# Kernel tuning notes

Measured on AMD Instinct MI355X. Metric: run time of the kernel, lower is better.

## Reference

```python
import jax, jax.numpy as jnp
import numpy as np

B, NQ, NK = 32, 1, 4096
Q_SIZE = K_SIZE = 512
H = 256


def setup_inputs() -> dict:
    key = jax.random.key(0)
    ks = jax.random.split(key, 6)
    return {
        "queries": jax.random.normal(ks[0], (B, NQ, Q_SIZE), jnp.float32),
        "keys": jax.random.normal(ks[1], (B, NK, K_SIZE), jnp.float32),
        "values": jax.random.normal(ks[2], (B, NK, 1), jnp.float32),
        "W_q": jax.random.normal(ks[3], (Q_SIZE, H), jnp.float32) / np.sqrt(Q_SIZE),
        "W_k": jax.random.normal(ks[4], (K_SIZE, H), jnp.float32) / np.sqrt(K_SIZE),
        "w_v": jax.random.normal(ks[5], (H,), jnp.float32) / np.sqrt(H),
    }


def reference(queries, keys, values, W_q, W_k, w_v):
    # Project queries and keys to hidden dim
    q = jnp.einsum("bqd,dh->bqh", queries, W_q)            # [B, NQ, H]
    k = jnp.einsum("bkd,dh->bkh", keys, W_k)               # [B, NK, H]
    # Broadcast-add + tanh: [B, NQ, NK, H]
    features = jnp.tanh(q[:, :, None, :] + k[:, None, :, :])
    # Reduce hidden dim with w_v -> scores [B, NQ, NK]
    scores = jnp.einsum("bqkh,h->bqk", features, w_v)
    attn = jax.nn.softmax(scores, axis=-1)                 # [B, NQ, NK]
    # Module squeezes n_q dim (==1) and trailing value dim (==1)
    return attn[:, 0, :] * values[:, :, 0]                 # [B, NK]
```

## Files before the change

kernel.cpp:

```cpp
#include <hip/hip_runtime.h>
#include <cstdint>
#include <cstddef>

#define NB 32
#define NKEYS 4096
#define DQ 512
#define HDIM 256

#define BM 64
#define BK 64

typedef __attribute__((ext_vector_type(8))) short bf16x8;
typedef __attribute__((ext_vector_type(4))) float f32x4;

typedef __attribute__((address_space(1))) const unsigned int g_u32;
typedef __attribute__((address_space(3))) unsigned int l_u32;

__device__ __forceinline__ unsigned short f2bf(float f) {
    union { float f; unsigned u; } v; v.f = f;
    unsigned r = v.u + 0x7FFFu + ((v.u >> 16) & 1u);
    return (unsigned short)(r >> 16);
}

__device__ __forceinline__ float tanh_fast(float x) {
    float e = __expf(2.0f * x);
    return 1.0f - 2.0f / (e + 1.0f);
}

__device__ __forceinline__ void gload_lds16(const void* g, void* l) {
    __builtin_amdgcn_global_load_lds((g_u32*)g, (l_u32*)l, 16, 0, 0);
}

__global__ void k_prep_wkT(const float* __restrict__ Wk, unsigned short* __restrict__ WkT) {
    __shared__ unsigned short t[64][65];
    const int tid = threadIdx.x;
    const int dt = (blockIdx.x >> 2) << 6;
    const int ht = (blockIdx.x & 3) << 6;
    #pragma unroll
    for (int i = 0; i < 16; ++i) {
        int idx = tid + i * 256;
        int d = idx >> 6, h = idx & 63;
        t[d][h] = f2bf(Wk[(size_t)(dt + d) * HDIM + ht + h]);
    }
    __syncthreads();
    #pragma unroll
    for (int i = 0; i < 16; ++i) {
        int idx = tid + i * 256;
        int h = idx >> 6, d = idx & 63;
        WkT[(size_t)(ht + h) * DQ + dt + d] = t[d][h];
    }
}

__global__ void k_qproj(const float* __restrict__ q, const float* __restrict__ Wq,
                        float* __restrict__ qp) {
    __shared__ float qrow[DQ];
    __shared__ float part[256];
    const int blk = blockIdx.x;
    const int b = blk >> 2, hq = blk & 3;
    const int tid = threadIdx.x;
    qrow[tid]       = q[b * DQ + tid];
    qrow[tid + 256] = q[b * DQ + tid + 256];
    __syncthreads();
    const int h = (hq << 6) + (tid & 63);
    const int d0 = (tid >> 6) << 7;
    float s = 0.f;
    #pragma unroll 4
    for (int d = d0; d < d0 + 128; ++d)
        s += qrow[d] * Wq[d * HDIM + h];
    part[tid] = s;
    __syncthreads();
    if (tid < 64)
        qp[b * HDIM + (hq << 6) + tid] =
            part[tid] + part[tid + 64] + part[tid + 128] + part[tid + 192];
}

__global__ __launch_bounds__(256, 2) void k_scores(
        const float* __restrict__ keys, const unsigned short* __restrict__ WkT,
        const float* __restrict__ qp, const float* __restrict__ wv,
        float* __restrict__ scores) {
    __shared__ __align__(16) unsigned short As[2][BM * BK];
    __shared__ __align__(16) unsigned short Bs[2][HDIM * BK];
    float* s_rows = reinterpret_cast<float*>(&As[0][0]);

    const int tid  = threadIdx.x;
    const int lane = tid & 63;
    const int wid  = tid >> 6;
    const int row0 = blockIdx.x * BM;
    const int b    = row0 >> 12;
    const int l15  = lane & 15;
    const int l4   = lane >> 4;

    const int ar  = tid >> 4;
    const int ac4 = tid & 15;
    const float* aptr[4];
    int awoff[4];
    #pragma unroll
    for (int i = 0; i < 4; ++i) {
        const int row = ar + i * 16;
        aptr[i]  = keys + (size_t)(row0 + row) * DQ + ac4 * 4;
        awoff[i] = row * 128 + (((ac4 >> 1) ^ (row & 7)) << 4) + (ac4 & 1) * 8;
    }
    const int bcol = wid * 64 + (lane >> 3);
    const int bsw  = (lane & 7) ^ ((lane >> 3) & 7);
    const unsigned short* bptr = WkT + (size_t)bcol * DQ + bsw * 8;

    const int r7 = l15 & 7;
    const int asl0 = (l4 ^ r7) << 4;
    const int asl1 = ((4 + l4) ^ r7) << 4;

    f32x4 acc[4][4];
    #pragma unroll
    for (int i = 0; i < 4; ++i)
        #pragma unroll
        for (int j = 0; j < 4; ++j)
            acc[i][j] = (f32x4){0.f, 0.f, 0.f, 0.f};

    float4 rA[4];

    #pragma unroll
    for (int i = 0; i < 4; ++i) rA[i] = *reinterpret_cast<const float4*>(aptr[i]);
    #pragma unroll
    for (int q = 0; q < 8; ++q)
        gload_lds16(bptr + q * (8 * DQ), &Bs[0][(wid * 64 + q * 8) * BK]);
    #pragma unroll
    for (int i = 0; i < 4; ++i) {
        ushort4 h4;
        h4.x = f2bf(rA[i].x); h4.y = f2bf(rA[i].y); h4.z = f2bf(rA[i].z); h4.w = f2bf(rA[i].w);
        *reinterpret_cast<ushort4*>(reinterpret_cast<char*>(&As[0][0]) + awoff[i]) = h4;
    }
    __syncthreads();

    #pragma unroll
    for (int kt = 0; kt < 8; ++kt) {
        const int cur = kt & 1;
        if (kt < 7) {
            #pragma unroll
            for (int i = 0; i < 4; ++i)
                rA[i] = *reinterpret_cast<const float4*>(aptr[i] + (kt + 1) * BK);
            #pragma unroll
            for (int q = 0; q < 8; ++q)
                gload_lds16(bptr + (kt + 1) * BK + q * (8 * DQ),
                            &Bs[cur ^ 1][(wid * 64 + q * 8) * BK]);
        }
        const char* Ab = reinterpret_cast<const char*>(&As[cur][0]);
        const char* Bb = reinterpret_cast<const char*>(&Bs[cur][0]);
        #pragma unroll
        for (int kk = 0; kk < 2; ++kk) {
            const int sl = kk ? asl1 : asl0;
            bf16x8 a[4], bb[4];
            #pragma unroll
            for (int i = 0; i < 4; ++i)
                a[i] = *reinterpret_cast<const bf16x8*>(Ab + (i * 16 + l15) * 128 + sl);
            #pragma unroll
            for (int j = 0; j < 4; ++j)
                bb[j] = *reinterpret_cast<const bf16x8*>(Bb + (wid * 64 + j * 16 + l15) * 128 + sl);
            #pragma unroll
            for (int i = 0; i < 4; ++i)
                #pragma unroll
                for (int j = 0; j < 4; ++j)
                    acc[i][j] = __builtin_amdgcn_mfma_f32_16x16x32_bf16(
                        a[i], bb[j], acc[i][j], 0, 0, 0);
        }
        __syncthreads();
        if (kt < 7) {
            #pragma unroll
            for (int i = 0; i < 4; ++i) {
                ushort4 h4;
                h4.x = f2bf(rA[i].x); h4.y = f2bf(rA[i].y);
                h4.z = f2bf(rA[i].z); h4.w = f2bf(rA[i].w);
                *reinterpret_cast<ushort4*>(
                    reinterpret_cast<char*>(&As[cur ^ 1][0]) + awoff[i]) = h4;
            }
            __syncthreads();
        }
    }

    if (tid < BM) s_rows[tid] = 0.f;
    __syncthreads();

    float qv[4], wvv[4];
    #pragma unroll
    for (int j = 0; j < 4; ++j) {
        int col = wid * 64 + j * 16 + l15;
        qv[j]  = qp[b * HDIM + col];
        wvv[j] = wv[col];
    }
    #pragma unroll
    for (int i = 0; i < 4; ++i) {
        #pragma unroll
        for (int r = 0; r < 4; ++r) {
            float p = 0.f;
            #pragma unroll
            for (int j = 0; j < 4; ++j) {
                float x = acc[i][j][r] + qv[j];
                p += tanh_fast(x) * wvv[j];
            }
            p += __shfl_xor(p, 1);
            p += __shfl_xor(p, 2);
            p += __shfl_xor(p, 4);
            p += __shfl_xor(p, 8);
            if (l15 == 0)
                atomicAdd(&s_rows[i * 16 + l4 * 4 + r], p);
        }
    }
    __syncthreads();
    if (tid < BM) scores[row0 + tid] = s_rows[tid];
}

__global__ void k_softmax(const float* __restrict__ scores, const float* __restrict__ values,
                          float* __restrict__ out) {
    __shared__ float red[32];
    const int b = blockIdx.x, tid = threadIdx.x;
    const float* s = scores + b * NKEYS;
    float v[4];
    float m = -1e30f;
    #pragma unroll
    for (int i = 0; i < 4; ++i) { v[i] = s[tid + i * 1024]; m = fmaxf(m, v[i]); }
    #pragma unroll
    for (int off = 1; off < 64; off <<= 1) m = fmaxf(m, __shfl_xor(m, off));
    const int w = tid >> 6;
    if ((tid & 63) == 0) red[w] = m;
    __syncthreads();
    m = red[0];
    #pragma unroll
    for (int i = 1; i < 16; ++i) m = fmaxf(m, red[i]);
    float sum = 0.f;
    #pragma unroll
    for (int i = 0; i < 4; ++i) { v[i] = __expf(v[i] - m); sum += v[i]; }
    #pragma unroll
    for (int off = 1; off < 64; off <<= 1) sum += __shfl_xor(sum, off);
    if ((tid & 63) == 0) red[16 + w] = sum;
    __syncthreads();
    sum = red[16];
    #pragma unroll
    for (int i = 1; i < 16; ++i) sum += red[16 + i];
    const float inv = 1.0f / sum;
    #pragma unroll
    for (int i = 0; i < 4; ++i) {
        int n = tid + i * 1024;
        out[b * NKEYS + n] = v[i] * inv * values[b * NKEYS + n];
    }
}

extern "C" void kernel_launch(void* const* d_in, const int* in_sizes, int n_in,
                              void* d_out, int out_size, void* d_ws, size_t ws_size,
                              hipStream_t stream) {
    const float* queries = (const float*)d_in[0];
    const float* keys    = (const float*)d_in[1];
    const float* values  = (const float*)d_in[2];
    const float* Wq      = (const float*)d_in[3];
    const float* Wk      = (const float*)d_in[4];
    const float* wv      = (const float*)d_in[5];
    float* out = (float*)d_out;

    char* ws = (char*)d_ws;
    float* scores        = (float*)ws;
    float* qp            = (float*)(ws + 131072 * 4);
    unsigned short* WkT  = (unsigned short*)(ws + 131072 * 4 + 8192 * 4);

    hipLaunchKernelGGL(k_prep_wkT, dim3(32),   dim3(256),  0, stream, Wk, WkT);
    hipLaunchKernelGGL(k_qproj,    dim3(128),  dim3(256),  0, stream, queries, Wq, qp);
    hipLaunchKernelGGL(k_scores,   dim3(NB * NKEYS / BM), dim3(256), 0, stream,
                       keys, WkT, qp, wv, scores);
    hipLaunchKernelGGL(k_softmax,  dim3(NB),   dim3(1024), 0, stream, scores, values, out);
}
```

Baseline: 414.6 us.

## Deepen key-tile prefetch to two stages and merge per-iteration barriers

The fp32 key loads are now issued two K-tiles ahead into alternating register buffers, so global-load latency overlaps with more MFMA work. The two __syncthreads per iteration become a single raw s_barrier preceded by explicit vmcnt/lgkmcnt waits, and the MFMA block is wrapped in s_setprio to favour the matrix issue. The change relies on hand-counted vmcnt values and on removing the barrier between the compute reads of As[cur] and the writes to As[nxt]. It also holds more live registers, which may lower occupancy.

```diff
diff --git a/kernel.cpp b/kernel.cpp
--- a/kernel.cpp
+++ b/kernel.cpp
@@ -115,32 +115,38 @@
         for (int j = 0; j < 4; ++j)
             acc[i][j] = (f32x4){0.f, 0.f, 0.f, 0.f};
 
-    float4 rA[4];
-
-    #pragma unroll
-    for (int i = 0; i < 4; ++i) rA[i] = *reinterpret_cast<const float4*>(aptr[i]);
+    float4 rA1[4], rA2[4];
+
     #pragma unroll
     for (int q = 0; q < 8; ++q)
         gload_lds16(bptr + q * (8 * DQ), &Bs[0][(wid * 64 + q * 8) * BK]);
-    #pragma unroll
-    for (int i = 0; i < 4; ++i) {
-        ushort4 h4;
-        h4.x = f2bf(rA[i].x); h4.y = f2bf(rA[i].y); h4.z = f2bf(rA[i].z); h4.w = f2bf(rA[i].w);
-        *reinterpret_cast<ushort4*>(reinterpret_cast<char*>(&As[0][0]) + awoff[i]) = h4;
-    }
-    __syncthreads();
+    {
+        float4 t0[4];
+        #pragma unroll
+        for (int i = 0; i < 4; ++i) t0[i] = *reinterpret_cast<const float4*>(aptr[i]);
+        #pragma unroll
+        for (int i = 0; i < 4; ++i) {
+            ushort4 h4;
+            h4.x = f2bf(t0[i].x); h4.y = f2bf(t0[i].y);
+            h4.z = f2bf(t0[i].z); h4.w = f2bf(t0[i].w);
+            *reinterpret_cast<ushort4*>(reinterpret_cast<char*>(&As[0][0]) + awoff[i]) = h4;
+        }
+    }
+    asm volatile("s_waitcnt vmcnt(0)" ::: "memory");
+    asm volatile("s_waitcnt lgkmcnt(0)" ::: "memory");
+    __builtin_amdgcn_s_barrier();
+    #pragma unroll
+    for (int i = 0; i < 4; ++i)
+        rA1[i] = *reinterpret_cast<const float4*>(aptr[i] + 1 * BK);
 
     #pragma unroll
     for (int kt = 0; kt < 8; ++kt) {
-        const int cur = kt & 1;
+        const int cur = kt & 1, nxt = cur ^ 1;
         if (kt < 7) {
-            #pragma unroll
-            for (int i = 0; i < 4; ++i)
-                rA[i] = *reinterpret_cast<const float4*>(aptr[i] + (kt + 1) * BK);
             #pragma unroll
             for (int q = 0; q < 8; ++q)
                 gload_lds16(bptr + (kt + 1) * BK + q * (8 * DQ),
-                            &Bs[cur ^ 1][(wid * 64 + q * 8) * BK]);
+                            &Bs[nxt][(wid * 64 + q * 8) * BK]);
         }
         const char* Ab = reinterpret_cast<const char*>(&As[cur][0]);
         const char* Bb = reinterpret_cast<const char*>(&Bs[cur][0]);
@@ -154,24 +160,36 @@
             #pragma unroll
             for (int j = 0; j < 4; ++j)
                 bb[j] = *reinterpret_cast<const bf16x8*>(Bb + (wid * 64 + j * 16 + l15) * 128 + sl);
+            __builtin_amdgcn_s_setprio(1);
             #pragma unroll
             for (int i = 0; i < 4; ++i)
                 #pragma unroll
                 for (int j = 0; j < 4; ++j)
                     acc[i][j] = __builtin_amdgcn_mfma_f32_16x16x32_bf16(
                         a[i], bb[j], acc[i][j], 0, 0, 0);
-        }
-        __syncthreads();
+            __builtin_amdgcn_s_setprio(0);
+        }
         if (kt < 7) {
             #pragma unroll
             for (int i = 0; i < 4; ++i) {
+                const float4 v = (kt & 1) ? rA2[i] : rA1[i];
                 ushort4 h4;
-                h4.x = f2bf(rA[i].x); h4.y = f2bf(rA[i].y);
-                h4.z = f2bf(rA[i].z); h4.w = f2bf(rA[i].w);
+                h4.x = f2bf(v.x); h4.y = f2bf(v.y); h4.z = f2bf(v.z); h4.w = f2bf(v.w);
                 *reinterpret_cast<ushort4*>(
-                    reinterpret_cast<char*>(&As[cur ^ 1][0]) + awoff[i]) = h4;
+                    reinterpret_cast<char*>(&As[nxt][0]) + awoff[i]) = h4;
             }
-            __syncthreads();
+            if (kt < 6) {
+                #pragma unroll
+                for (int i = 0; i < 4; ++i) {
+                    const float4 v = *reinterpret_cast<const float4*>(aptr[i] + (kt + 2) * BK);
+                    if (kt & 1) rA1[i] = v; else rA2[i] = v;
+                }
+                asm volatile("s_waitcnt vmcnt(4)" ::: "memory");
+            } else {
+                asm volatile("s_waitcnt vmcnt(0)" ::: "memory");
+            }
+            asm volatile("s_waitcnt lgkmcnt(0)" ::: "memory");
+            __builtin_amdgcn_s_barrier();
         }
     }
 
```

After: 398.9 us. 3.8% less time.
